# Kernel tuning notes

Hardware: AMD Instinct MI355X
Metric: run time of the kernel (lower is better)

## Reference

```python
import jax, jax.numpy as jnp
import numpy as np

IN_DIM = 1024
HID = 1024
DEPTH = 13            # perfect binary tree: 2**13 = 8192 leaves, 8191 internal nodes
N_LEAVES = 2 ** DEPTH
N_TOKENS = 8192
N_OPS = 4             # '+', '/', '*', '-' (ordered_op=False)


def setup_inputs() -> dict:
    key = jax.random.key(0)
    ks = jax.random.split(key, 16)
    sW = 1.0 / np.sqrt(IN_DIM)
    sU = 1.0 / np.sqrt(HID)
    inp = {
        "tokens": jax.random.normal(ks[0], (N_TOKENS, IN_DIM), jnp.float32),
        "leaf_token_ids": jax.random.randint(ks[1], (N_LEAVES,), 0, N_TOKENS),
        "op_ids": jax.random.randint(ks[2], (N_LEAVES - 1,), 0, N_OPS),
        "W_i": jax.random.normal(ks[3], (HID, IN_DIM), jnp.float32) * sW,
        "W_o": jax.random.normal(ks[4], (HID, IN_DIM), jnp.float32) * sW,
        "W_u": jax.random.normal(ks[5], (HID, IN_DIM), jnp.float32) * sW,
        "W_f": jax.random.normal(ks[6], (HID, IN_DIM), jnp.float32) * sW,
        "U_i": jax.random.normal(ks[7], (HID, HID), jnp.float32) * sU,
        "U_o": jax.random.normal(ks[8], (HID, HID), jnp.float32) * sU,
        "U_u": jax.random.normal(ks[9], (HID, HID), jnp.float32) * sU,
        "U_f": jax.random.normal(ks[10], (HID, HID), jnp.float32) * sU,
        "b_i": jnp.zeros((1, HID), jnp.float32),
        "b_o": jnp.zeros((1, HID), jnp.float32),
        "b_u": jnp.zeros((1, HID), jnp.float32),
        "b_f": jnp.zeros((1, HID), jnp.float32),
        "op_emb": jax.random.uniform(ks[11], (N_OPS, IN_DIM), jnp.float32, -1.0, 1.0),
        "c_init": jnp.zeros((2, HID), jnp.float32),
        "h_init": jnp.zeros((2, HID), jnp.float32),
    }
    return inp


def reference(tokens, leaf_token_ids, op_ids, W_i, W_o, W_u, W_f,
              U_i, U_o, U_u, U_f, b_i, b_o, b_u, b_f,
              op_emb, c_init, h_init):
    """Depth-batched Child-Sum TreeLSTM over a perfect binary tree.
    op_ids are stored root-first level order: level l (root=0) occupies
    op_ids[2**l - 1 : 2**(l+1) - 1]. Leaves are level DEPTH.
    Children of node j at level l are nodes 2j, 2j+1 at level l+1.
    Returns jnp.stack([c_root, h_root])  -> [2, 1, HID]."""
    H = U_i.shape[0]

    def node_step(x, c_state, h_state):
        # x: [n, in_dim]; c_state/h_state: [n, 2, H]
        h_sum = h_state.sum(axis=1)                                   # [n, H]
        i = jax.nn.sigmoid(x @ W_i.T + h_sum @ U_i.T + b_i)
        o = jax.nn.sigmoid(x @ W_o.T + h_sum @ U_o.T + b_o)
        u = jnp.tanh(x @ W_u.T + h_sum @ U_u.T + b_u)
        f = jax.nn.sigmoid((x @ W_f.T)[:, None, :] + h_state @ U_f.T + b_f)  # [n,2,H]
        c = i * u + (f * c_state).sum(axis=1)                         # [n, H]
        h = o * jnp.tanh(c)
        return c, h

    n = leaf_token_ids.shape[0]
    depth = int(np.log2(n))
    # leaves: learnable init states, x = embedding of the token
    x = tokens[leaf_token_ids]                                        # [n, in_dim]
    c, h = node_step(x,
                     jnp.broadcast_to(c_init, (n, 2, H)),
                     jnp.broadcast_to(h_init, (n, 2, H)))
    # internal levels, bottom-up
    for l in range(depth - 1, -1, -1):
        m = 2 ** l
        off = m - 1
        x = op_emb[op_ids[off:off + m]]                               # [m, in_dim]
        c, h = node_step(x, c.reshape(m, 2, H), h.reshape(m, 2, H))
    return jnp.stack([c, h])  # [2, 1, H]: root (c, h)
```

## Files before the change

kernel.cpp:

```cpp
#include <hip/hip_runtime.h>

typedef unsigned short u16;
typedef __attribute__((ext_vector_type(4))) unsigned short us4;
typedef __attribute__((ext_vector_type(4))) float f4;
typedef __attribute__((ext_vector_type(8))) short bf16x8;
typedef __attribute__((ext_vector_type(4))) float f32x4;

__device__ __forceinline__ u16 f2bf(float x) {
  unsigned u = __float_as_uint(x);
  return (u16)((u + 0x7FFFu + ((u >> 16) & 1u)) >> 16);
}
__device__ __forceinline__ float b2f(u16 s) {
  return __uint_as_float(((unsigned)s) << 16);
}
__device__ __forceinline__ float sigm(float x) { return 1.f / (1.f + __expf(-x)); }
__device__ __forceinline__ float tanhf_(float x) { return 2.f / (1.f + __expf(-2.f * x)) - 1.f; }

__global__ void setup_kernel(
    const float* __restrict__ tokens, const int* __restrict__ leaf_ids,
    const float* __restrict__ w0, const float* __restrict__ w1,
    const float* __restrict__ w2, const float* __restrict__ w3,
    const float* __restrict__ u0, const float* __restrict__ u1,
    const float* __restrict__ u2, const float* __restrict__ u3,
    const float* __restrict__ b0, const float* __restrict__ b1,
    const float* __restrict__ b2, const float* __restrict__ b3,
    const float* __restrict__ op_emb, const float* __restrict__ h_init,
    u16* __restrict__ Wb, u16* __restrict__ Ub, u16* __restrict__ Xl,
    float* __restrict__ xw, float* __restrict__ leafC) {
  const int bid = blockIdx.x;
  if (bid < 8192) {
    int mat = bid >> 10;
    int off4 = (int)(bid & 1023) * 256 + threadIdx.x;
    const float* src; u16* dst;
    switch (mat) {
      case 0: src = w0; dst = Wb; break;
      case 1: src = w1; dst = Wb + 1048576; break;
      case 2: src = w2; dst = Wb + 2097152; break;
      case 3: src = w3; dst = Wb + 3145728; break;
      case 4: src = u0; dst = Ub; break;
      case 5: src = u1; dst = Ub + 1048576; break;
      case 6: src = u2; dst = Ub + 2097152; break;
      default: src = u3; dst = Ub + 3145728; break;
    }
    f4 v = ((const f4*)src)[off4];
    us4 o = {f2bf(v[0]), f2bf(v[1]), f2bf(v[2]), f2bf(v[3])};
    ((us4*)dst)[off4] = o;
  } else if (bid < 16384) {
    int n = bid - 8192, t = threadIdx.x;
    int tok = leaf_ids[n];
    f4 v = ((const f4*)(tokens + (size_t)tok * 1024))[t];
    us4 o = {f2bf(v[0]), f2bf(v[1]), f2bf(v[2]), f2bf(v[3])};
    ((us4*)(Xl + (size_t)n * 1024))[t] = o;
  } else {
    const int wave = threadIdx.x >> 6, lane = threadIdx.x & 63;
    const int wid = (bid - 16384) * 4 + wave;
    const f4* xr;
    const f4* wr;
    float bias;
    bool dual = false;
    const f4* xr2 = nullptr;
    float* dst;
    if (wid < 16384) {
      int op = wid >> 12, g = (wid >> 10) & 3, j = wid & 1023;
      const float* wsrc; const float* bs;
      switch (g) {
        case 0: wsrc = w0; bs = b0; break;
        case 1: wsrc = w1; bs = b1; break;
        case 2: wsrc = w2; bs = b2; break;
        default: wsrc = w3; bs = b3; break;
      }
      xr = (const f4*)(op_emb + (size_t)op * 1024);
      wr = (const f4*)(wsrc + (size_t)j * 1024);
      bias = bs[j];
      dst = xw + wid;
    } else {
      int id2 = wid - 16384;
      int sel = id2 >> 10, j = id2 & 1023;
      const f4* h0 = (const f4*)h_init;
      const f4* h1 = (const f4*)(h_init + 1024);
      if (sel < 3) {
        const float* usrc; const float* bs;
        switch (sel) {
          case 0: usrc = u0; bs = b0; break;
          case 1: usrc = u1; bs = b1; break;
          default: usrc = u2; bs = b2; break;
        }
        xr = h0; xr2 = h1; dual = true;
        wr = (const f4*)(usrc + (size_t)j * 1024);
        bias = bs[j];
      } else {
        xr = (sel == 3) ? h0 : h1;
        wr = (const f4*)(u3 + (size_t)j * 1024);
        bias = b3[j];
      }
      dst = leafC + id2;
    }
    float s = 0.f;
#pragma unroll
    for (int i = 0; i < 4; ++i) {
      int k = lane + 64 * i;
      f4 a = xr[k];
      if (dual) {
        f4 a2 = xr2[k];
        a[0] += a2[0]; a[1] += a2[1]; a[2] += a2[2]; a[3] += a2[3];
      }
      f4 b = wr[k];
      s += a[0] * b[0] + a[1] * b[1] + a[2] * b[2] + a[3] * b[3];
    }
#pragma unroll
    for (int off = 32; off > 0; off >>= 1) s += __shfl_xor(s, off);
    if (lane == 0) *dst = s + bias;
  }
}

template <int NRT, int NCT>
__global__ __launch_bounds__(256, (NRT == 8 ? 2 : 3)) void tree_gemm(
    const u16* __restrict__ A, const u16* __restrict__ Wm,
    const float* __restrict__ consts,
    const int* __restrict__ ops,
    const float* __restrict__ c_in,
    float* __restrict__ c_out, u16* __restrict__ h_out,
    int nrows, int m_parents, int is_leaf, float* __restrict__ out_root) {
  constexpr int ROWS = NRT * 16;
  constexpr int COLS = NCT * 16;
  constexpr int S = 64 / NCT;
  constexpr int LOG2S = (NCT == 2 ? 5 : 4);
  constexpr int NST = NRT / 2;
  constexpr int DBUF = NRT * 2048;
  constexpr int PASSES = (NRT == 8 ? 4 : (NRT == 4 ? 2 : 1));
  constexpr int RPP = ROWS / PASSES;
  constexpr int FPP = RPP / 16;
  constexpr int SMEM_U16 =
      (4 * RPP * 68 > NRT * 2048 ? 4 * RPP * 68 : NRT * 2048);
  __shared__ __align__(16) u16 smem[SMEM_U16];
  char* smem_c = (char*)smem;

  const int tid = threadIdx.x;
  const int wave = tid >> 6;
  const int lane = tid & 63;
  const int stripe = blockIdx.x & (S - 1);
  const int rowblk = blockIdx.x >> LOG2S;
  const int r0 = rowblk * ROWS;
  const int j0 = stripe * COLS;
  const int ln15 = lane & 15, quad = lane >> 4;
  const int sub = lane >> 3, gsel = lane & 7;

  const char* pAsrc[NST];
  unsigned a_dst[NST];
#pragma unroll
  for (int i = 0; i < NST; ++i) {
    int slot = (wave * NST + i) * 8 + sub;
    int row = r0 + slot; if (row >= nrows) row = nrows - 1;
    pAsrc[i] = (const char*)(A + (size_t)row * 1024 + (unsigned)((gsel ^ sub) * 8));
    a_dst[i] = (unsigned)((wave * NST + i) * 1024 + lane * 16);
  }
  const char* pB[NCT];
#pragma unroll
  for (int f = 0; f < NCT; ++f)
    pB[f] = (const char*)(Wm + (size_t)(wave * 1024 + j0 + f * 16 + ln15) * 1024 + quad * 8);

  unsigned a_base[2];
#pragma unroll
  for (int ks = 0; ks < 2; ++ks)
    a_base[ks] = (unsigned)(ln15 * 128 + (((ks * 4 + quad) ^ (ln15 & 7)) * 16));

  f32x4 acc[NRT][NCT];
#pragma unroll
  for (int t = 0; t < NRT; ++t)
#pragma unroll
    for (int f = 0; f < NCT; ++f) acc[t][f] = (f32x4){0.f, 0.f, 0.f, 0.f};

#pragma unroll
  for (int i = 0; i < NST; ++i)
    __builtin_amdgcn_global_load_lds(
        (const __attribute__((address_space(1))) void*)(pAsrc[i]),
        (__attribute__((address_space(3))) void*)(smem_c + a_dst[i]), 16, 0, 0);
  bf16x8 bcur[2][NCT], bnxt[2][NCT];
#pragma unroll
  for (int ks = 0; ks < 2; ++ks)
#pragma unroll
    for (int f = 0; f < NCT; ++f)
      bcur[ks][f] = *(const bf16x8*)(pB[f] + ks * 64);

#pragma unroll
  for (int ch = 0; ch < 16; ++ch) {
    __syncthreads();
    if (ch < 15) {
#pragma unroll
      for (int i = 0; i < NST; ++i)
        __builtin_amdgcn_global_load_lds(
            (const __attribute__((address_space(1))) void*)(pAsrc[i] + (ch + 1) * 128),
            (__attribute__((address_space(3))) void*)(smem_c + ((ch + 1) & 1) * DBUF + a_dst[i]),
            16, 0, 0);
    }
    const unsigned cb = (unsigned)((ch & 1) * DBUF);
    {
      bf16x8 af[NRT];
#pragma unroll
      for (int t = 0; t < NRT; ++t)
        af[t] = *(const bf16x8*)(smem_c + cb + a_base[0] + t * 2048);
#pragma unroll
      for (int t = 0; t < NRT; ++t)
#pragma unroll
        for (int f = 0; f < NCT; ++f)
          acc[t][f] = __builtin_amdgcn_mfma_f32_16x16x32_bf16(af[t], bcur[0][f],
                                                              acc[t][f], 0, 0, 0);
    }
    if (ch < 15) {
#pragma unroll
      for (int ks = 0; ks < 2; ++ks)
#pragma unroll
        for (int f = 0; f < NCT; ++f)
          bnxt[ks][f] = *(const bf16x8*)(pB[f] + (ch + 1) * 128 + ks * 64);
    }
    {
      bf16x8 af[NRT];
#pragma unroll
      for (int t = 0; t < NRT; ++t)
        af[t] = *(const bf16x8*)(smem_c + cb + a_base[1] + t * 2048);
#pragma unroll
      for (int t = 0; t < NRT; ++t)
#pragma unroll
        for (int f = 0; f < NCT; ++f)
          acc[t][f] = __builtin_amdgcn_mfma_f32_16x16x32_bf16(af[t], bcur[1][f],
                                                              acc[t][f], 0, 0, 0);
    }
#pragma unroll
    for (int ks = 0; ks < 2; ++ks)
#pragma unroll
      for (int f = 0; f < NCT; ++f) bcur[ks][f] = bnxt[ks][f];
  }

#pragma unroll
  for (int pass = 0; pass < PASSES; ++pass) {
    __syncthreads();
#pragma unroll
    for (int tt = 0; tt < FPP; ++tt) {
      int t = pass * FPP + tt;
#pragma unroll
      for (int f = 0; f < NCT; ++f)
#pragma unroll
        for (int k = 0; k < 4; ++k) {
          int row = tt * 16 + quad * 4 + k;
          int col = f * 16 + ln15;
          smem[(wave * RPP + row) * 68 + col] = f2bf(acc[t][f][k]);
        }
    }
    __syncthreads();
    const int rbase = r0 + pass * RPP;

    if (is_leaf) {
      for (int e = tid; e < RPP * COLS; e += 256) {
        int r = e / COLS, j = e % COLS;
        int col = j0 + j, n = rbase + r;
        float p0 = b2f(smem[(0 * RPP + r) * 68 + j]);
        float p1 = b2f(smem[(1 * RPP + r) * 68 + j]);
        float p2 = b2f(smem[(2 * RPP + r) * 68 + j]);
        float p3 = b2f(smem[(3 * RPP + r) * 68 + j]);
        float i_ = sigm(p0 + consts[col]);
        float o_ = sigm(p1 + consts[1024 + col]);
        float u_ = tanhf_(p2 + consts[2048 + col]);
        float f0 = sigm(p3 + consts[3072 + col]);
        float f1 = sigm(p3 + consts[4096 + col]);
        float c = i_ * u_ + f0 * c_in[col] + f1 * c_in[1024 + col];
        float h = o_ * tanhf_(c);
        c_out[(size_t)n * 1024 + col] = c;
        h_out[(size_t)n * 1024 + col] = f2bf(h);
      }
    } else {
      for (int e = tid; e < (RPP / 2) * COLS; e += 256) {
        int p = e / COLS, j = e % COLS;
        int np = (rbase >> 1) + p;
        if (np >= m_parents) break;
        int col = j0 + j;
        int op = ops[np];
        const float* xwop = consts + ((unsigned)(op * 4) << 10);
        float p0a = b2f(smem[(0 * RPP + 2 * p) * 68 + j]), p0b = b2f(smem[(0 * RPP + 2 * p + 1) * 68 + j]);
        float p1a = b2f(smem[(1 * RPP + 2 * p) * 68 + j]), p1b = b2f(smem[(1 * RPP + 2 * p + 1) * 68 + j]);
        float p2a = b2f(smem[(2 * RPP + 2 * p) * 68 + j]), p2b = b2f(smem[(2 * RPP + 2 * p + 1) * 68 + j]);
        float p3a = b2f(smem[(3 * RPP + 2 * p) * 68 + j]), p3b = b2f(smem[(3 * RPP + 2 * p + 1) * 68 + j]);
        float i_ = sigm(p0a + p0b + xwop[col]);
        float o_ = sigm(p1a + p1b + xwop[1024 + col]);
        float u_ = tanhf_(p2a + p2b + xwop[2048 + col]);
        float f0 = sigm(p3a + xwop[3072 + col]);
        float f1 = sigm(p3b + xwop[3072 + col]);
        float c = i_ * u_ + f0 * c_in[(size_t)(rbase + 2 * p) * 1024 + col]
                          + f1 * c_in[(size_t)(rbase + 2 * p + 1) * 1024 + col];
        float h = o_ * tanhf_(c);
        if (m_parents == 1) {
          out_root[col] = c;
          out_root[1024 + col] = h;
        } else {
          c_out[(size_t)np * 1024 + col] = c;
          h_out[(size_t)np * 1024 + col] = f2bf(h);
        }
      }
    }
  }
}

__global__ __launch_bounds__(256, 2) void small_gemm(
    const u16* __restrict__ A, const u16* __restrict__ Um,
    const float* __restrict__ xw, const int* __restrict__ ops,
    const float* __restrict__ c_in,
    float* __restrict__ c_out, u16* __restrict__ h_out,
    int nrows, int m_parents, float* __restrict__ out_root) {
  __shared__ __align__(16) u16 smem[32768];
  char* smem_c = (char*)smem;
  const int tid = threadIdx.x;
  const int wave = tid >> 6, lane = tid & 63;
  const int stripe = blockIdx.x & 31, rowblk = blockIdx.x >> 5;
  const int r0 = rowblk * 32, j0 = stripe * 32;
  const int ln15 = lane & 15, quad = lane >> 4;
  const int sub = lane >> 3, gsel = lane & 7;

#pragma unroll
  for (int i = 0; i < 16; ++i) {
    int w = wave * 16 + i;
    int ch = w >> 2;
    int row = r0 + (w & 3) * 8 + sub;
    if (row >= nrows) row = nrows - 1;
    const char* src = (const char*)(A + (size_t)row * 1024 + (unsigned)(ch * 64) + (unsigned)((gsel ^ sub) * 8));
    __builtin_amdgcn_global_load_lds(
        (const __attribute__((address_space(1))) void*)src,
        (__attribute__((address_space(3))) void*)(smem_c + w * 1024 + lane * 16), 16, 0, 0);
  }
  const char* pB[2];
#pragma unroll
  for (int f = 0; f < 2; ++f)
    pB[f] = (const char*)(Um + (size_t)(wave * 1024 + j0 + f * 16 + ln15) * 1024 + quad * 8);
  unsigned a_base[2];
#pragma unroll
  for (int ks = 0; ks < 2; ++ks)
    a_base[ks] = (unsigned)(ln15 * 128 + (((ks * 4 + quad) ^ (ln15 & 7)) * 16));

  f32x4 acc[2][2];
#pragma unroll
  for (int t = 0; t < 2; ++t)
#pragma unroll
    for (int f = 0; f < 2; ++f) acc[t][f] = (f32x4){0.f, 0.f, 0.f, 0.f};

  __syncthreads();

#pragma unroll
  for (int ch = 0; ch < 16; ++ch) {
    bf16x8 b[2][2];
#pragma unroll
    for (int ks = 0; ks < 2; ++ks)
#pragma unroll
      for (int f = 0; f < 2; ++f)
        b[ks][f] = *(const bf16x8*)(pB[f] + ch * 128 + ks * 64);
#pragma unroll
    for (int ks = 0; ks < 2; ++ks) {
      bf16x8 af[2];
#pragma unroll
      for (int t = 0; t < 2; ++t)
        af[t] = *(const bf16x8*)(smem_c + ch * 4096 + a_base[ks] + t * 2048);
#pragma unroll
      for (int t = 0; t < 2; ++t)
#pragma unroll
        for (int f = 0; f < 2; ++f)
          acc[t][f] = __builtin_amdgcn_mfma_f32_16x16x32_bf16(af[t], b[ks][f], acc[t][f], 0, 0, 0);
    }
  }

  __syncthreads();
#pragma unroll
  for (int t = 0; t < 2; ++t)
#pragma unroll
    for (int f = 0; f < 2; ++f)
#pragma unroll
      for (int k = 0; k < 4; ++k) {
        int row = t * 16 + quad * 4 + k;
        int col = f * 16 + ln15;
        smem[(wave * 32 + row) * 68 + col] = f2bf(acc[t][f][k]);
      }
  __syncthreads();
  for (int e = tid; e < 16 * 32; e += 256) {
    int p = e >> 5, j = e & 31;
    int np = (r0 >> 1) + p;
    if (np >= m_parents) break;
    int col = j0 + j;
    int op = ops[np];
    const float* xwop = xw + ((unsigned)op << 12);
    float p0a = b2f(smem[(0 * 32 + 2 * p) * 68 + j]), p0b = b2f(smem[(0 * 32 + 2 * p + 1) * 68 + j]);
    float p1a = b2f(smem[(1 * 32 + 2 * p) * 68 + j]), p1b = b2f(smem[(1 * 32 + 2 * p + 1) * 68 + j]);
    float p2a = b2f(smem[(2 * 32 + 2 * p) * 68 + j]), p2b = b2f(smem[(2 * 32 + 2 * p + 1) * 68 + j]);
    float p3a = b2f(smem[(3 * 32 + 2 * p) * 68 + j]), p3b = b2f(smem[(3 * 32 + 2 * p + 1) * 68 + j]);
    float i_ = sigm(p0a + p0b + xwop[col]);
    float o_ = sigm(p1a + p1b + xwop[1024 + col]);
    float u_ = tanhf_(p2a + p2b + xwop[2048 + col]);
    float f0 = sigm(p3a + xwop[3072 + col]);
    float f1 = sigm(p3b + xwop[3072 + col]);
    float c = i_ * u_ + f0 * c_in[(size_t)(r0 + 2 * p) * 1024 + col]
                      + f1 * c_in[(size_t)(r0 + 2 * p + 1) * 1024 + col];
    float h = o_ * tanhf_(c);
    if (m_parents == 1) {
      out_root[col] = c;
      out_root[1024 + col] = h;
    } else {
      c_out[(size_t)np * 1024 + col] = c;
      h_out[(size_t)np * 1024 + col] = f2bf(h);
    }
  }
}

extern "C" void kernel_launch(void* const* d_in, const int* in_sizes, int n_in,
                              void* d_out, int out_size, void* d_ws, size_t ws_size,
                              hipStream_t stream) {
  const float* tokens = (const float*)d_in[0];
  const int* leaf_ids = (const int*)d_in[1];
  const int* op_ids = (const int*)d_in[2];
  const float* W0 = (const float*)d_in[3];
  const float* W1 = (const float*)d_in[4];
  const float* W2 = (const float*)d_in[5];
  const float* W3 = (const float*)d_in[6];
  const float* U0 = (const float*)d_in[7];
  const float* U1 = (const float*)d_in[8];
  const float* U2 = (const float*)d_in[9];
  const float* U3 = (const float*)d_in[10];
  const float* B0 = (const float*)d_in[11];
  const float* B1 = (const float*)d_in[12];
  const float* B2 = (const float*)d_in[13];
  const float* B3 = (const float*)d_in[14];
  const float* op_emb = (const float*)d_in[15];
  const float* c_init = (const float*)d_in[16];
  const float* h_init = (const float*)d_in[17];
  float* out = (float*)d_out;

  char* ws = (char*)d_ws;
  u16* Wb = (u16*)ws;
  u16* Ub = Wb + (size_t)4 * 1024 * 1024;
  u16* Xl = Ub + (size_t)4 * 1024 * 1024;
  u16* hA = Xl + (size_t)8192 * 1024;
  u16* hB = hA + (size_t)8192 * 1024;
  float* cA = (float*)(hB + (size_t)4096 * 1024);
  float* cB = cA + (size_t)8192 * 1024;
  float* xw = cB + (size_t)4096 * 1024;
  float* lc = xw + 16 * 1024;

  setup_kernel<<<21760, 256, 0, stream>>>(tokens, leaf_ids,
                                          W0, W1, W2, W3, U0, U1, U2, U3,
                                          B0, B1, B2, B3, op_emb, h_init,
                                          Wb, Ub, Xl, xw, lc);

  tree_gemm<8, 2><<<64 * 32, 256, 0, stream>>>(Xl, Wb, lc, nullptr, c_init,
                                               cA, hA, 8192, 0, 1, out);

  const u16* hin = hA; const float* cin = cA;
  u16* hout = hB; float* cout = cB;
  for (int l = 12; l >= 0; --l) {
    int m = 1 << l;
    int nrows = 2 * m;
    if (nrows >= 2048) {
      tree_gemm<8, 2><<<(nrows / 128) * 32, 256, 0, stream>>>(
          hin, Ub, xw, op_ids + (m - 1), cin, cout, hout, nrows, m, 0, out);
    } else if (nrows >= 1024) {
      tree_gemm<4, 2><<<(nrows / 64) * 32, 256, 0, stream>>>(
          hin, Ub, xw, op_ids + (m - 1), cin, cout, hout, nrows, m, 0, out);
    } else {
      int rg = nrows / 32; if (rg < 1) rg = 1;
      small_gemm<<<rg * 32, 256, 0, stream>>>(
          hin, Ub, xw, op_ids + (m - 1), cin, cout, hout, nrows, m, out);
    }
    const u16* th = hin; hin = hout; hout = (u16*)th;
    const float* tc = cin; cin = cout; cout = (float*)tc;
  }
}
```

Measured before the change: 551.1 us.

## Precompute child h sums and use split-level GEMM for upper tree levels

```diff
diff --git a/kernel.cpp b/kernel.cpp
--- a/kernel.cpp
+++ b/kernel.cpp
@@ -120,7 +120,8 @@
     const int* __restrict__ ops,
     const float* __restrict__ c_in,
     float* __restrict__ c_out, u16* __restrict__ h_out,
-    int nrows, int m_parents, int is_leaf, float* __restrict__ out_root) {
+    int nrows, int m_parents, int is_leaf, float* __restrict__ out_root,
+    u16* __restrict__ hs_out) {
   constexpr int ROWS = NRT * 16;
   constexpr int COLS = NCT * 16;
   constexpr int S = 64 / NCT;
@@ -266,6 +267,10 @@
         float h = o_ * tanhf_(c);
         c_out[(size_t)n * 1024 + col] = c;
         h_out[(size_t)n * 1024 + col] = f2bf(h);
+        if (hs_out) {
+          float hp = h + __shfl_xor(h, 32);
+          if (lane < 32) hs_out[(size_t)(n >> 1) * 1024 + col] = f2bf(hp);
+        }
       }
     } else {
       for (int e = tid; e < (RPP / 2) * COLS; e += 256) {
@@ -295,6 +300,213 @@
           h_out[(size_t)np * 1024 + col] = f2bf(h);
         }
       }
+    }
+  }
+}
+
+__device__ constexpr int JG[4][5] = {{0,0,0,0,1},{1,1,1,2,2},{2,2,3,3,3},{3,3,3,3,3}};
+__device__ constexpr int JT[4][5] = {{0,1,2,3,0},{1,2,3,0,1},{2,3,0,1,2},{3,4,5,6,7}};
+__device__ constexpr int SL[4][5] = {{0,0,0,0,1},{0,0,0,1,1},{0,0,1,1,1},{0,0,0,0,0}};
+__device__ constexpr int NSLOT[4]  = {2,2,2,1};
+__device__ constexpr int GSLOT[4][2] = {{0,1},{1,2},{2,3},{3,3}};
+
+struct WState {
+  bf16x8 bcur[2][2][2];
+  bf16x8 bnxt[2][2][2];
+  f32x4 acc[5][2];
+  const char* pB[2][2];
+};
+
+template <int W>
+__device__ __forceinline__ void sl_init(WState& S, const u16* Um, int j0,
+                                        int ln15, int quad) {
+#pragma unroll
+  for (int s = 0; s < NSLOT[W]; ++s) {
+    const int g = GSLOT[W][s];
+#pragma unroll
+    for (int fr = 0; fr < 2; ++fr)
+      S.pB[s][fr] = (const char*)(Um + (size_t)(g * 1024 + j0 + fr * 16 + ln15) * 1024 + quad * 8);
+  }
+#pragma unroll
+  for (int j = 0; j < 5; ++j)
+#pragma unroll
+    for (int fr = 0; fr < 2; ++fr) S.acc[j][fr] = (f32x4){0.f, 0.f, 0.f, 0.f};
+#pragma unroll
+  for (int s = 0; s < NSLOT[W]; ++s)
+#pragma unroll
+    for (int ks = 0; ks < 2; ++ks)
+#pragma unroll
+      for (int fr = 0; fr < 2; ++fr)
+        S.bcur[ks][s][fr] = *(const bf16x8*)(S.pB[s][fr] + ks * 64);
+}
+
+template <int W>
+__device__ __forceinline__ void sl_chunk(WState& S, const char* cb,
+                                         unsigned ab0, unsigned ab1, int ch) {
+  {
+    bf16x8 af[5];
+#pragma unroll
+    for (int j = 0; j < 5; ++j) {
+      const int tb = (JG[W][j] < 3 ? JT[W][j] * 2048 : 8192 + JT[W][j] * 2048);
+      af[j] = *(const bf16x8*)(cb + tb + ab0);
+    }
+#pragma unroll
+    for (int j = 0; j < 5; ++j)
+#pragma unroll
+      for (int fr = 0; fr < 2; ++fr)
+        S.acc[j][fr] = __builtin_amdgcn_mfma_f32_16x16x32_bf16(
+            af[j], S.bcur[0][SL[W][j]][fr], S.acc[j][fr], 0, 0, 0);
+  }
+  if (ch < 15) {
+#pragma unroll
+    for (int s = 0; s < NSLOT[W]; ++s)
+#pragma unroll
+      for (int ks = 0; ks < 2; ++ks)
+#pragma unroll
+        for (int fr = 0; fr < 2; ++fr)
+          S.bnxt[ks][s][fr] = *(const bf16x8*)(S.pB[s][fr] + (ch + 1) * 128 + ks * 64);
+  }
+  {
+    bf16x8 af[5];
+#pragma unroll
+    for (int j = 0; j < 5; ++j) {
+      const int tb = (JG[W][j] < 3 ? JT[W][j] * 2048 : 8192 + JT[W][j] * 2048);
+      af[j] = *(const bf16x8*)(cb + tb + ab1);
+    }
+#pragma unroll
+    for (int j = 0; j < 5; ++j)
+#pragma unroll
+      for (int fr = 0; fr < 2; ++fr)
+        S.acc[j][fr] = __builtin_amdgcn_mfma_f32_16x16x32_bf16(
+            af[j], S.bcur[1][SL[W][j]][fr], S.acc[j][fr], 0, 0, 0);
+  }
+#pragma unroll
+  for (int s = 0; s < NSLOT[W]; ++s)
+#pragma unroll
+    for (int ks = 0; ks < 2; ++ks)
+#pragma unroll
+      for (int fr = 0; fr < 2; ++fr) S.bcur[ks][s][fr] = S.bnxt[ks][s][fr];
+}
+
+template <int W>
+__device__ __forceinline__ void sl_epiw(WState& S, u16* smem, int ln15, int quad) {
+#pragma unroll
+  for (int j = 0; j < 5; ++j) {
+    const int rbase = (JG[W][j] < 3 ? JG[W][j] * 64 + JT[W][j] * 16
+                                    : 192 + JT[W][j] * 16);
+#pragma unroll
+    for (int fr = 0; fr < 2; ++fr)
+#pragma unroll
+      for (int k = 0; k < 4; ++k) {
+        int row = rbase + quad * 4 + k;
+        int col = fr * 16 + ln15;
+        smem[row * 68 + col] = f2bf(S.acc[j][fr][k]);
+      }
+  }
+}
+
+__global__ __launch_bounds__(256, 2) void splitlvl_gemm(
+    const u16* __restrict__ Hs,
+    const u16* __restrict__ Hc,
+    const u16* __restrict__ Um, const float* __restrict__ xw,
+    const int* __restrict__ ops, const float* __restrict__ c_in,
+    float* __restrict__ c_out, u16* __restrict__ h_out,
+    u16* __restrict__ hs_out, int m) {
+  __shared__ __align__(16) u16 smem[24576];
+  char* smem_c = (char*)smem;
+  const int tid = threadIdx.x;
+  const int wave = tid >> 6, lane = tid & 63;
+  const int stripe = blockIdx.x & 31;
+  const int rowblk = blockIdx.x >> 5;
+  const int r0 = rowblk * 64;
+  const int j0 = stripe * 32;
+  const int ln15 = lane & 15, quad = lane >> 4;
+  const int sub = lane >> 3, gsel = lane & 7;
+
+  const char* pAsrc[6];
+  unsigned a_dst[6];
+#pragma unroll
+  for (int i = 0; i < 6; ++i) {
+    int g = wave * 6 + i;
+    const u16* base;
+    int row;
+    if (g < 8) {
+      row = r0 + g * 8 + sub;
+      if (row >= m) row = m - 1;
+      base = Hs;
+    } else {
+      row = 2 * r0 + (g - 8) * 8 + sub;
+      if (row >= 2 * m) row = 2 * m - 1;
+      base = Hc;
+    }
+    pAsrc[i] = (const char*)(base + (size_t)row * 1024 + (unsigned)((gsel ^ sub) * 8));
+    a_dst[i] = (unsigned)(g * 1024 + lane * 16);
+  }
+  unsigned a_base[2];
+#pragma unroll
+  for (int ks = 0; ks < 2; ++ks)
+    a_base[ks] = (unsigned)(ln15 * 128 + (((ks * 4 + quad) ^ (ln15 & 7)) * 16));
+
+  WState S;
+  switch (wave) {
+    case 0: sl_init<0>(S, Um, j0, ln15, quad); break;
+    case 1: sl_init<1>(S, Um, j0, ln15, quad); break;
+    case 2: sl_init<2>(S, Um, j0, ln15, quad); break;
+    default: sl_init<3>(S, Um, j0, ln15, quad); break;
+  }
+#pragma unroll
+  for (int i = 0; i < 6; ++i)
+    __builtin_amdgcn_global_load_lds(
+        (const __attribute__((address_space(1))) void*)(pAsrc[i]),
+        (__attribute__((address_space(3))) void*)(smem_c + a_dst[i]), 16, 0, 0);
+
+#pragma unroll
+  for (int ch = 0; ch < 16; ++ch) {
+    __syncthreads();
+    if (ch < 15) {
+#pragma unroll
+      for (int i = 0; i < 6; ++i)
+        __builtin_amdgcn_global_load_lds(
+            (const __attribute__((address_space(1))) void*)(pAsrc[i] + (ch + 1) * 128),
+            (__attribute__((address_space(3))) void*)(smem_c + ((ch + 1) & 1) * 24576 + a_dst[i]),
+            16, 0, 0);
+    }
+    const char* cb = smem_c + (ch & 1) * 24576;
+    switch (wave) {
+      case 0: sl_chunk<0>(S, cb, a_base[0], a_base[1], ch); break;
+      case 1: sl_chunk<1>(S, cb, a_base[0], a_base[1], ch); break;
+      case 2: sl_chunk<2>(S, cb, a_base[0], a_base[1], ch); break;
+      default: sl_chunk<3>(S, cb, a_base[0], a_base[1], ch); break;
+    }
+  }
+
+  __syncthreads();
+  switch (wave) {
+    case 0: sl_epiw<0>(S, smem, ln15, quad); break;
+    case 1: sl_epiw<1>(S, smem, ln15, quad); break;
+    case 2: sl_epiw<2>(S, smem, ln15, quad); break;
+    default: sl_epiw<3>(S, smem, ln15, quad); break;
+  }
+  __syncthreads();
+  for (int e = tid; e < 64 * 32; e += 256) {
+    int p = e >> 5, j = e & 31;
+    int P = r0 + p;
+    int col = j0 + j;
+    int op = ops[P];
+    const float* xwop = xw + ((unsigned)op << 12);
+    float i_ = sigm(b2f(smem[(0 + p) * 68 + j]) + xwop[col]);
+    float o_ = sigm(b2f(smem[(64 + p) * 68 + j]) + xwop[1024 + col]);
+    float u_ = tanhf_(b2f(smem[(128 + p) * 68 + j]) + xwop[2048 + col]);
+    float f0 = sigm(b2f(smem[(192 + 2 * p) * 68 + j]) + xwop[3072 + col]);
+    float f1 = sigm(b2f(smem[(192 + 2 * p + 1) * 68 + j]) + xwop[3072 + col]);
+    float c = i_ * u_ + f0 * c_in[(size_t)(2 * P) * 1024 + col]
+                      + f1 * c_in[(size_t)(2 * P + 1) * 1024 + col];
+    float h = o_ * tanhf_(c);
+    c_out[(size_t)P * 1024 + col] = c;
+    h_out[(size_t)P * 1024 + col] = f2bf(h);
+    if (hs_out) {
+      float hp = h + __shfl_xor(h, 32);
+      if (lane < 32) hs_out[(size_t)(P >> 1) * 1024 + col] = f2bf(hp);
     }
   }
 }
@@ -438,6 +650,9 @@
   float* cB = cA + (size_t)8192 * 1024;
   float* xw = cB + (size_t)4096 * 1024;
   float* lc = xw + 16 * 1024;
+  const bool split_ok = ws_size >= (size_t)118 * 1024 * 1024;
+  u16* hsA = (u16*)(ws + (size_t)105 * 1024 * 1024);
+  u16* hsB = (u16*)(ws + (size_t)113 * 1024 * 1024);
 
   setup_kernel<<<21760, 256, 0, stream>>>(tokens, leaf_ids,
                                           W0, W1, W2, W3, U0, U1, U2, U3,
@@ -445,19 +660,26 @@
                                           Wb, Ub, Xl, xw, lc);
 
   tree_gemm<8, 2><<<64 * 32, 256, 0, stream>>>(Xl, Wb, lc, nullptr, c_init,
-                                               cA, hA, 8192, 0, 1, out);
+                                               cA, hA, 8192, 0, 1, out,
+                                               split_ok ? hsA : nullptr);
 
   const u16* hin = hA; const float* cin = cA;
   u16* hout = hB; float* cout = cB;
+  u16* hs_cur = hsA; u16* hs_nxt = hsB;
   for (int l = 12; l >= 0; --l) {
     int m = 1 << l;
     int nrows = 2 * m;
-    if (nrows >= 2048) {
+    if (l >= 9 && split_ok) {
+      splitlvl_gemm<<<(m / 64) * 32, 256, 0, stream>>>(
+          hs_cur, hin, Ub, xw, op_ids + (m - 1), cin, cout, hout,
+          (l > 9) ? hs_nxt : nullptr, m);
+      u16* th = hs_cur; hs_cur = hs_nxt; hs_nxt = th;
+    } else if (nrows >= 2048) {
       tree_gemm<8, 2><<<(nrows / 128) * 32, 256, 0, stream>>>(
-          hin, Ub, xw, op_ids + (m - 1), cin, cout, hout, nrows, m, 0, out);
+          hin, Ub, xw, op_ids + (m - 1), cin, cout, hout, nrows, m, 0, out, nullptr);
     } else if (nrows >= 1024) {
       tree_gemm<4, 2><<<(nrows / 64) * 32, 256, 0, stream>>>(
-          hin, Ub, xw, op_ids + (m - 1), cin, cout, hout, nrows, m, 0, out);
+          hin, Ub, xw, op_ids + (m - 1), cin, cout, hout, nrows, m, 0, out, nullptr);
     } else {
       int rg = nrows / 32; if (rg < 1) rg = 1;
       small_gemm<<<rg * 32, 256, 0, stream>>>(
```

Measured after the change: 639.1 us. 1.16x slower.
